# Performance work log

Hardware: AMD Instinct MI355X
Metric: run time of the kernel (lower is better)

## Reference

```python
import jax, jax.numpy as jnp
import numpy as np

HEADS, DIM_HEAD, LANDMARKS, PINV_ITERS = 8, 64, 256, 6


def moore_penrose_pinv(x, iters=PINV_ITERS):
    abs_x = jnp.abs(x)
    col = abs_x.sum(-1)
    row = abs_x.sum(-2)
    z = jnp.swapaxes(x, -1, -2) / (jnp.max(col) * jnp.max(row))
    I = jnp.eye(x.shape[-1], dtype=x.dtype)
    for _ in range(iters):
        xz = x @ z
        z = 0.25 * z @ (13 * I - xz @ (15 * I - xz @ (7 * I - xz)))
    return z


def nystrom_attention(x, w_qkv, w_out, b_out, res_conv_w):
    b, n, dim = x.shape
    m = LANDMARKS
    pad = (m - n % m) % m
    x = jnp.pad(x, ((0, 0), (pad, 0), (0, 0)))  # pad at front like F.pad(x,(0,0,pad,0))
    npad = n + pad
    qkv = x @ w_qkv  # (b, npad, 3*heads*dim_head)
    q, k, v = jnp.split(qkv, 3, axis=-1)
    sh = lambda t: t.reshape(b, npad, HEADS, DIM_HEAD).transpose(0, 2, 1, 3)
    q, k, v = sh(q), sh(k), sh(v)  # (b,h,npad,dh)
    q = q * (DIM_HEAD ** -0.5)
    l = npad // m
    q_l = q.reshape(b, HEADS, m, l, DIM_HEAD).mean(axis=3)  # landmarks (b,h,m,dh)
    k_l = k.reshape(b, HEADS, m, l, DIM_HEAD).mean(axis=3)
    attn1 = jax.nn.softmax(jnp.einsum('bhid,bhjd->bhij', q, k_l), -1)   # (b,h,npad,m)
    attn2 = jax.nn.softmax(jnp.einsum('bhid,bhjd->bhij', q_l, k_l), -1)  # (b,h,m,m)
    attn3 = jax.nn.softmax(jnp.einsum('bhid,bhjd->bhij', q_l, k), -1)   # (b,h,m,npad)
    out = attn1 @ (moore_penrose_pinv(attn2) @ (attn3 @ v))  # (b,h,npad,dh)
    # depthwise residual conv over sequence dim (Conv2d(heads,heads,(33,1),groups=heads,bias=False))
    res = jax.lax.conv_general_dilated(v, res_conv_w, (1, 1), ((16, 16), (0, 0)),
                                       dimension_numbers=('NCHW', 'OIHW', 'NCHW'),
                                       feature_group_count=HEADS)
    out = out + res
    out = out.transpose(0, 2, 1, 3).reshape(b, npad, HEADS * DIM_HEAD)
    out = out @ w_out + b_out
    return out[:, -n:]


def camil_forward(bag, adj_row, adj_col, adj_val, w_qkv, w_out, b_out, res_conv_w,
                  wq, wk, wv_w, wv_b, v_att, u_att, w_att, fc_kernel, fc_bias):
    N = bag.shape[1]
    # encoder
    xg = nystrom_attention(bag, w_qkv, w_out, b_out, res_conv_w)[0]  # (N,D)
    enc = xg + bag  # (1,N,D)
    q = enc @ wq  # (1,N,256)
    k = enc @ wk
    attn = jnp.einsum('bnd,bmd->bnm', q, k)[0] / jnp.sqrt(jnp.float32(256.0))  # (N,N)
    # sparse adjacency-masked neighbor aggregation
    edge_scores = adj_val * attn[adj_row, adj_col]
    A_raw = jax.ops.segment_sum(edge_scores, adj_row, num_segments=N)  # (N,)
    alpha = jax.nn.softmax(A_raw)
    value = bag @ wv_w + wv_b  # (1,N,D)
    xl = alpha[:, None] * value  # (1,N,D)
    wei2 = jax.nn.sigmoid(-xl) ** 2
    xo = xl * 2 * wei2 + 2 * enc * (1 - wei2)  # (1,N,D)
    # gated MIL attention (softmax over dim 0 of size 1, as in original)
    inst = jnp.tanh(xo @ v_att) * jax.nn.sigmoid(xo @ u_att)
    scores = inst @ w_att  # (1,N,1)
    k_alpha = jax.nn.softmax(scores, axis=0)
    attn_output = k_alpha * xo
    pooled = attn_output[0].sum(axis=0, keepdims=True)  # (1,D)
    out = pooled @ fc_kernel + fc_bias  # (1,1)
    return out, A_raw, k_alpha


def setup_inputs() -> dict:
    key = jax.random.key(0)
    ks = jax.random.split(key, 16)
    N, D, E = 10000, 512, 90000
    s = 0.02
    return {
        'bag': jax.random.normal(ks[0], (1, N, D), jnp.float32),
        'adj_row': jax.random.randint(ks[1], (E,), 0, N),
        'adj_col': jax.random.randint(ks[2], (E,), 0, N),
        'adj_val': jax.random.uniform(ks[3], (E,), jnp.float32),
        'w_qkv': jax.random.normal(ks[4], (D, 3 * HEADS * DIM_HEAD), jnp.float32) * s,
        'w_out': jax.random.normal(ks[5], (HEADS * DIM_HEAD, D), jnp.float32) * s,
        'b_out': jnp.zeros((D,), jnp.float32),
        'res_conv_w': jax.random.normal(ks[6], (HEADS, 1, 33, 1), jnp.float32) * s,
        'wq': jax.random.normal(ks[7], (D, 256), jnp.float32) * s,
        'wk': jax.random.normal(ks[8], (D, 256), jnp.float32) * s,
        'wv_w': jax.random.normal(ks[9], (D, D), jnp.float32) * s,
        'wv_b': jnp.zeros((D,), jnp.float32),
        'v_att': jax.random.normal(ks[10], (D, 128), jnp.float32) * s,
        'u_att': jax.random.normal(ks[11], (D, 128), jnp.float32) * s,
        'w_att': jax.random.normal(ks[12], (128, 1), jnp.float32) * s,
        'fc_kernel': jax.random.normal(ks[13], (D, 1), jnp.float32) * s,
        'fc_bias': jnp.zeros((1,), jnp.float32),
    }


def reference(bag, adj_row, adj_col, adj_val, w_qkv, w_out, b_out, res_conv_w,
              wq, wk, wv_w, wv_b, v_att, u_att, w_att, fc_kernel, fc_bias):
    return camil_forward(bag, adj_row, adj_col, adj_val, w_qkv, w_out, b_out, res_conv_w,
                         wq, wk, wv_w, wv_b, v_att, u_att, w_att, fc_kernel, fc_bias)
```

## Files before the change

kernel.cpp:

```cpp
#include <hip/hip_runtime.h>
#include <hip/hip_bf16.h>
#include <math.h>

#define NSEQ   10000
#define NPAD   10240
#define PADR   240
#define HEADS  8
#define DH     64
#define LM     256
#define LFAC   40
#define DMODEL 512
#define DQK    256
#define OUTSZ  20001
#define NSPLIT 16
#define KCH    128

typedef __attribute__((ext_vector_type(8))) short bf16x8;
typedef __attribute__((ext_vector_type(4))) float f32x4;
#define MFMA16(a,b,c) __builtin_amdgcn_mfma_f32_16x16x32_bf16(a,b,c,0,0,0)

typedef __attribute__((address_space(1))) const unsigned char gconst_t;
typedef __attribute__((address_space(3))) unsigned char lds_t;
#define GLD16(gp, lp) __builtin_amdgcn_global_load_lds((gconst_t*)(gp), (lds_t*)(lp), 16, 0, 0)

__device__ __forceinline__ float b2f(ushort u) {
    return __uint_as_float(((unsigned)u) << 16);
}
__device__ __forceinline__ ushort f2b(float f) {
    unsigned u = __float_as_uint(f);
    unsigned r = (u + 0x7FFFu + ((u >> 16) & 1u)) >> 16;
    return (ushort)r;
}
__device__ __forceinline__ unsigned fenc(float f) {
    unsigned u = __float_as_uint(f);
    return (u & 0x80000000u) ? ~u : (u | 0x80000000u);
}
__device__ __forceinline__ float fdec(unsigned k) {
    return __uint_as_float((k & 0x80000000u) ? (k & 0x7FFFFFFFu) : ~k);
}
__device__ __forceinline__ int swz8(int bid, int nwg) {
    int q = nwg >> 3, r = nwg & 7;
    int x = bid & 7, idx = bid >> 3;
    int start = (x < r) ? x * (q + 1) : r * (q + 1) + (x - r) * q;
    return start + idx;
}
__device__ __forceinline__ f32x4 tr4(f32x4 v, int p) {
    f32x4 u, w;
    float s, r;
    s = (p & 1) ? v[0] : v[1]; r = __shfl_xor(s, 1);
    u[0] = (p & 1) ? r : v[0]; u[1] = (p & 1) ? v[1] : r;
    s = (p & 1) ? v[2] : v[3]; r = __shfl_xor(s, 1);
    u[2] = (p & 1) ? r : v[2]; u[3] = (p & 1) ? v[3] : r;
    s = (p & 2) ? u[0] : u[2]; r = __shfl_xor(s, 2);
    w[0] = (p & 2) ? r : u[0]; w[2] = (p & 2) ? u[2] : r;
    s = (p & 2) ? u[1] : u[3]; r = __shfl_xor(s, 2);
    w[1] = (p & 2) ? r : u[1]; w[3] = (p & 2) ? u[3] : r;
    return w;
}

__global__ __launch_bounds__(256)
void cvtw_k(const float* __restrict__ in, ushort* __restrict__ out,
            float* __restrict__ outbuf, const float* __restrict__ fcb,
            unsigned int* __restrict__ mx,
            const float* __restrict__ w_qkv, const float* __restrict__ w_out,
            const float* __restrict__ wq, const float* __restrict__ wk,
            const float* __restrict__ wv_w,
            ushort* __restrict__ wqkvT, ushort* __restrict__ woutT,
            ushort* __restrict__ wqkT)
{
    __shared__ float tile[32][33];
    int bid = blockIdx.x;
    if (bid < 5000) {
        int i = bid * 256 + threadIdx.x;
        float4 v = ((const float4*)in)[i];
        ushort4 u; u.x = f2b(v.x); u.y = f2b(v.y); u.z = f2b(v.z); u.w = f2b(v.w);
        ((ushort4*)out)[i] = u;
        if (i == 0) {
            outbuf[0] = fcb[0];
            mx[0] = 0u; mx[1] = 0u;
            mx[2] = 0u;
            ((float*)mx)[3] = 0.f;
        }
        if (i >= 1 && i <= NSEQ) outbuf[i] = 0.f;
        if (i >= NSEQ + 1 && i < OUTSZ) outbuf[i] = 1.0f;
    } else {
        int wb = bid - 5000;
        int g0 = (wb % 96) * 32, r0 = (wb / 96) * 32;
        const float* src; ushort* outp; int C; int lc0;
        if (g0 < 1536)      { src = w_qkv; outp = wqkvT;                      C = 1536; lc0 = g0; }
        else if (g0 < 2048) { src = w_out; outp = woutT;                      C = 512;  lc0 = g0 - 1536; }
        else if (g0 < 2304) { src = wq;    outp = wqkT;                       C = 256;  lc0 = g0 - 2048; }
        else if (g0 < 2560) { src = wk;    outp = wqkT + 256*512;             C = 256;  lc0 = g0 - 2304; }
        else                { src = wv_w;  outp = wqkvT + (size_t)1536*512;   C = 512;  lc0 = g0 - 2560; }
        int tx = threadIdx.x & 31, ty = threadIdx.x >> 5;
        for (int i = ty; i < 32; i += 8) tile[i][tx] = src[(size_t)(r0 + i) * C + lc0 + tx];
        __syncthreads();
        for (int i = ty; i < 32; i += 8) outp[(size_t)(lc0 + i) * 512 + r0 + tx] = f2b(tile[tx][i]);
    }
}

template<int MODE, int TN>
__global__ __launch_bounds__(256)
void mgemm(const ushort* __restrict__ A, const ushort* __restrict__ Bt,
           int Mlog, int N, int K, int padr, int nbx,
           void* __restrict__ P0, void* __restrict__ P1, void* __restrict__ P2,
           void* __restrict__ P3, void* __restrict__ P4,
           const float* __restrict__ bias, const ushort* __restrict__ extra)
{
    constexpr int NF = TN / 32;
    constexpr int BSB = TN * 64;
    __shared__ __align__(16) char As[2 * 8192];
    __shared__ __align__(16) char Bs[2 * BSB];
    const int tid = threadIdx.x;
    const int l = tid & 63, w = tid >> 6;
    const int wm = w >> 1, wn = w & 1;
    const int wk_ = swz8(blockIdx.x, gridDim.x);
    const int row0 = (wk_ / nbx) * 128, col0 = (wk_ % nbx) * TN;
    const int lr = l & 15, lg = l >> 4;
    const bool slow = (MODE == 0) && (row0 < padr);
    const int NT = K >> 5;
    f32x4 acc[4][NF];
    #pragma unroll
    for (int i = 0; i < 4; ++i)
        #pragma unroll
        for (int j = 0; j < NF; ++j) acc[i][j] = (f32x4){0.f, 0.f, 0.f, 0.f};

    auto stage = [&](int bf, int t) {
        int k0 = t << 5;
        if (!slow) {
            #pragma unroll
            for (int c = 0; c < 2; ++c) {
                int q = w * 2 + c;
                int row = q * 16 + (l >> 2);
                GLD16(A + (size_t)(row0 + row - padr) * K + k0 + (l & 3) * 8,
                      As + bf * 8192 + q * 1024);
            }
            if (TN == 128) {
                #pragma unroll
                for (int c = 0; c < 2; ++c) {
                    int q = w * 2 + c;
                    int row = q * 16 + (l >> 2);
                    GLD16(Bt + (size_t)(col0 + row) * K + k0 + (l & 3) * 8,
                          Bs + bf * BSB + q * 1024);
                }
            } else {
                int row = w * 16 + (l >> 2);
                GLD16(Bt + (size_t)(col0 + row) * K + k0 + (l & 3) * 8,
                      Bs + bf * BSB + w * 1024);
            }
        } else {
            #pragma unroll
            for (int c = 0; c < 2; ++c) {
                int gidx = c * 256 + tid;
                int row = gidx >> 2, gr = gidx & 3;
                int phys = row0 + row - padr;
                uint4 v = {0, 0, 0, 0};
                if (phys >= 0 && phys < Mlog - padr)
                    v = *(const uint4*)(A + (size_t)phys * K + k0 + gr * 8);
                *(uint4*)(As + bf * 8192 + gidx * 16) = v;
            }
            if (TN == 128) {
                #pragma unroll
                for (int c = 0; c < 2; ++c) {
                    int gidx = c * 256 + tid;
                    int row = gidx >> 2, gr = gidx & 3;
                    *(uint4*)(Bs + bf * BSB + gidx * 16) =
                        *(const uint4*)(Bt + (size_t)(col0 + row) * K + k0 + gr * 8);
                }
            } else {
                int row = tid >> 2, gr = tid & 3;
                *(uint4*)(Bs + bf * BSB + tid * 16) =
                    *(const uint4*)(Bt + (size_t)(col0 + row) * K + k0 + gr * 8);
            }
        }
    };

    int cur = 0;
    stage(0, 0);
    __syncthreads();
    for (int t = 0; t < NT; ++t) {
        if (t + 1 < NT) stage(cur ^ 1, t + 1);
        const char* Ab = As + cur * 8192;
        const char* Bb = Bs + cur * BSB;
        bf16x8 af[4];
        #pragma unroll
        for (int mf = 0; mf < 4; ++mf)
            af[mf] = *(const bf16x8*)(Ab + (wm * 64 + mf * 16 + lr) * 64 + lg * 16);
        #pragma unroll
        for (int nf = 0; nf < NF; ++nf) {
            bf16x8 bfr = *(const bf16x8*)(Bb + (wn * (TN / 2) + nf * 16 + lr) * 64 + lg * 16);
            #pragma unroll
            for (int mf = 0; mf < 4; ++mf)
                acc[mf][nf] = MFMA16(af[mf], bfr, acc[mf][nf]);
        }
        __syncthreads();
        cur ^= 1;
    }

    const int p = lr & 3;
    #pragma unroll
    for (int mf = 0; mf < 4; ++mf)
    #pragma unroll
    for (int nf = 0; nf < NF; ++nf) {
        int cb   = col0 + wn * (TN / 2) + nf * 16 + (lr & 12);
        int rowT = row0 + wm * 64 + mf * 16 + lg * 4 + p;
        if (MODE == 0) {
            int c = col0 + wn * (TN / 2) + nf * 16 + lr;
            if ((c >> 9) == 2) {
                int hh = (c >> 6) & 7;
                int kt  = (row0 + wm * 64 + mf * 16 + lg * 4) >> 5;
                int lgp = ((mf * 2) + (lg >> 1)) & 3;
                int lanep = lr + lgp * 16;
                int e0 = (lg & 1) * 4;
                ushort4 pk;
                pk.x = f2b(acc[mf][nf][0]); pk.y = f2b(acc[mf][nf][1]);
                pk.z = f2b(acc[mf][nf][2]); pk.w = f2b(acc[mf][nf][3]);
                *(ushort4*)&((ushort*)P3)[(((size_t)hh * (NPAD/32) + kt) * 4 + (nf & 3)) * 512
                                          + lanep * 8 + e0] = pk;
            }
            int t = cb >> 9;
            f32x4 v = acc[mf][nf];
            if (t == 0) { v[0] *= 0.125f; v[1] *= 0.125f; v[2] *= 0.125f; v[3] *= 0.125f; }
            f32x4 wv = tr4(v, p);
            ushort4 pk;
            pk.x = f2b(wv[0]); pk.y = f2b(wv[1]); pk.z = f2b(wv[2]); pk.w = f2b(wv[3]);
            if (t < 3) {
                int hh = (cb >> 6) & 7, d0 = cb & 63;
                ushort* dst = (t == 0) ? (ushort*)P0 : (t == 1) ? (ushort*)P1 : (ushort*)P2;
                *(ushort4*)&dst[((size_t)hh * NPAD + rowT) * DH + d0] = pk;
            } else {
                int phys = rowT - PADR;
                if (phys >= 0)
                    *(ushort4*)&((ushort*)P4)[(size_t)phys * DMODEL + (cb & 511)] = pk;
            }
        } else if (MODE == 1) {
            f32x4 wv = tr4(acc[mf][nf], p);
            if (rowT < Mlog) {
                float4 bi = *(const float4*)(bias + cb);
                ushort4 bg = *(const ushort4*)(extra + (size_t)rowT * N + cb);
                float o0 = wv[0] + bi.x + b2f(bg.x), o1 = wv[1] + bi.y + b2f(bg.y);
                float o2 = wv[2] + bi.z + b2f(bg.z), o3 = wv[3] + bi.w + b2f(bg.w);
                ushort4 pk; pk.x = f2b(o0); pk.y = f2b(o1); pk.z = f2b(o2); pk.w = f2b(o3);
                *(ushort4*)&((ushort*)P1)[(size_t)rowT * N + cb] = pk;
            }
        } else if (MODE == 6) {
            f32x4 wv = tr4(acc[mf][nf], p);
            if (rowT < Mlog) {
                ushort4 pk;
                pk.x = f2b(wv[0]); pk.y = f2b(wv[1]); pk.z = f2b(wv[2]); pk.w = f2b(wv[3]);
                if (cb < 256)
                    *(ushort4*)&((ushort*)P0)[(size_t)rowT * 256 + cb] = pk;
                else
                    *(ushort4*)&((ushort*)P1)[(size_t)rowT * 256 + (cb - 256)] = pk;
            }
        }
    }
}

template<bool PLAIN, bool BCI, bool WPK>
__global__ __launch_bounds__(256)
void pinv_k(const ushort* __restrict__ A, const ushort* __restrict__ Bt,
            int N, float cval, float scale,
            ushort* __restrict__ P0, ushort* __restrict__ P1)
{
    __shared__ __align__(16) char smem[49152];
    char* As = smem;
    char* Bs = smem + 16384;
    const int tid = threadIdx.x, l = tid & 63, w = tid >> 6;
    const int lr = l & 15, lg = l >> 4;
    const int col0 = blockIdx.x * 64, row0 = blockIdx.y * 32, h = blockIdx.z;
    const ushort* Ab = A + (size_t)h * 65536;
    const ushort* Btb = Bt + (size_t)h * ((size_t)N * 256);
    {
        int row = tid >> 3, seg = (tid & 7) * 64;
        const uint4* sa = (const uint4*)(Ab + (size_t)(row0 + row) * 256) + (tid & 7) * 4;
        #pragma unroll
        for (int e = 0; e < 4; ++e) {
            int off = (row * 512 + seg + e * 16) ^ ((row & 7) << 4);
            *(uint4*)(As + off) = sa[e];
        }
    }
    {
        int row = tid >> 2, seg = (tid & 3) * 128;
        const uint4* sb = (const uint4*)(Btb + (size_t)(col0 + row) * 256) + (tid & 3) * 8;
        int gn = col0 + row;
        #pragma unroll
        for (int e = 0; e < 8; ++e) {
            int off = (row * 512 + seg + e * 16) ^ ((row & 7) << 4);
            uint4 vb = sb[e];
            if (BCI) {
                union { uint4 u; ushort s[8]; } t; t.u = vb;
                int gk0 = (seg >> 1) + e * 8;
                #pragma unroll
                for (int j = 0; j < 8; ++j)
                    t.s[j] = f2b(((gn == gk0 + j) ? cval : 0.f) - b2f(t.s[j]));
                vb = t.u;
            }
            *(uint4*)(Bs + off) = vb;
        }
    }
    __syncthreads();
    f32x4 acc[2];
    acc[0] = (f32x4){0.f, 0.f, 0.f, 0.f};
    acc[1] = (f32x4){0.f, 0.f, 0.f, 0.f};
    #pragma unroll
    for (int ks = 0; ks < 8; ++ks) {
        bf16x8 af[2];
        #pragma unroll
        for (int mf = 0; mf < 2; ++mf) {
            int ar = mf * 16 + lr;
            af[mf] = *(const bf16x8*)(As + ((ar * 512 + ks * 64 + lg * 16) ^ ((ar & 7) << 4)));
        }
        int br = w * 16 + lr;
        bf16x8 bf = *(const bf16x8*)(Bs + ((br * 512 + ks * 64 + lg * 16) ^ ((br & 7) << 4)));
        acc[0] = MFMA16(af[0], bf, acc[0]);
        acc[1] = MFMA16(af[1], bf, acc[1]);
    }
    #pragma unroll
    for (int mf = 0; mf < 2; ++mf) {
        int r0v = row0 + mf * 16 + lg * 4;
        int c = col0 + w * 16 + lr;
        if (PLAIN) {
            #pragma unroll
            for (int i = 0; i < 4; ++i)
                P0[(size_t)h * 256 * N + (size_t)(r0v + i) * N + c] = f2b(acc[mf][i] * scale);
        }
        ushort4 pk;
        pk.x = f2b(acc[mf][0] * scale); pk.y = f2b(acc[mf][1] * scale);
        pk.z = f2b(acc[mf][2] * scale); pk.w = f2b(acc[mf][3] * scale);
        if (WPK) {
            int off = (((c >> 4) * 8 + (r0v >> 5)) << 9) + (((r0v >> 3) & 3) << 7)
                    + ((c & 15) << 3) + (r0v & 4);
            *(ushort4*)&P1[(size_t)h * 16384 + off] = pk;
        } else {
            *(ushort4*)&P1[(size_t)h * ((size_t)N * 256) + (size_t)c * 256 + r0v] = pk;
        }
    }
}

__global__ __launch_bounds__(256)
void ns2_k(const ushort* __restrict__ P, const ushort* __restrict__ Pt,
           const ushort* __restrict__ Z,
           ushort* __restrict__ Qt, ushort* __restrict__ V1)
{
    __shared__ __align__(16) char smem[49152];
    char* As = smem;
    char* Bs = smem + 16384;
    const int tid = threadIdx.x, l = tid & 63, w = tid >> 6;
    const int lr = l & 15, lg = l >> 4;
    const int col0 = blockIdx.x * 64;
    const int which = blockIdx.y >> 3;
    const int row0 = (blockIdx.y & 7) * 32;
    const int h = blockIdx.z;
    const ushort* Ab = (which ? Z : P) + (size_t)h * 65536;
    const ushort* Btb = Pt + (size_t)h * 65536;
    {
        int row = tid >> 3, seg = (tid & 7) * 64;
        const uint4* sa = (const uint4*)(Ab + (size_t)(row0 + row) * 256) + (tid & 7) * 4;
        #pragma unroll
        for (int e = 0; e < 4; ++e) {
            int off = (row * 512 + seg + e * 16) ^ ((row & 7) << 4);
            *(uint4*)(As + off) = sa[e];
        }
    }
    {
        int row = tid >> 2, seg = (tid & 3) * 128;
        const uint4* sb = (const uint4*)(Btb + (size_t)(col0 + row) * 256) + (tid & 3) * 8;
        int gn = col0 + row;
        #pragma unroll
        for (int e = 0; e < 8; ++e) {
            int off = (row * 512 + seg + e * 16) ^ ((row & 7) << 4);
            uint4 vb = sb[e];
            if (which == 0) {
                union { uint4 u; ushort s[8]; } t; t.u = vb;
                int gk0 = (seg >> 1) + e * 8;
                #pragma unroll
                for (int j = 0; j < 8; ++j)
                    t.s[j] = f2b(((gn == gk0 + j) ? 7.f : 0.f) - b2f(t.s[j]));
                vb = t.u;
            }
            *(uint4*)(Bs + off) = vb;
        }
    }
    __syncthreads();
    f32x4 acc[2];
    acc[0] = (f32x4){0.f, 0.f, 0.f, 0.f};
    acc[1] = (f32x4){0.f, 0.f, 0.f, 0.f};
    #pragma unroll
    for (int ks = 0; ks < 8; ++ks) {
        bf16x8 af[2];
        #pragma unroll
        for (int mf = 0; mf < 2; ++mf) {
            int ar = mf * 16 + lr;
            af[mf] = *(const bf16x8*)(As + ((ar * 512 + ks * 64 + lg * 16) ^ ((ar & 7) << 4)));
        }
        int br = w * 16 + lr;
        bf16x8 bf = *(const bf16x8*)(Bs + ((br * 512 + ks * 64 + lg * 16) ^ ((br & 7) << 4)));
        acc[0] = MFMA16(af[0], bf, acc[0]);
        acc[1] = MFMA16(af[1], bf, acc[1]);
    }
    #pragma unroll
    for (int mf = 0; mf < 2; ++mf) {
        int r0v = row0 + mf * 16 + lg * 4;
        int c = col0 + w * 16 + lr;
        if (which == 0) {
            ushort4 pk;
            pk.x = f2b(acc[mf][0]); pk.y = f2b(acc[mf][1]);
            pk.z = f2b(acc[mf][2]); pk.w = f2b(acc[mf][3]);
            *(ushort4*)&Qt[(size_t)h * 65536 + (size_t)c * 256 + r0v] = pk;
        } else {
            #pragma unroll
            for (int i = 0; i < 4; ++i)
                V1[(size_t)h * 65536 + (size_t)(r0v + i) * 256 + c] = f2b(acc[mf][i]);
        }
    }
}

__global__ __launch_bounds__(256)
void ns3_k(const ushort* __restrict__ V1, const ushort* __restrict__ Qt,
           const ushort* __restrict__ Z,
           ushort* __restrict__ Zn, ushort* __restrict__ Znt)
{
    __shared__ __align__(16) char smem[49152];
    char* As = smem;
    char* Bs = smem + 16384;
    const int tid = threadIdx.x, l = tid & 63, w = tid >> 6;
    const int lr = l & 15, lg = l >> 4;
    const int col0 = blockIdx.x * 64, row0 = blockIdx.y * 32, h = blockIdx.z;
    const ushort* Ab = V1 + (size_t)h * 65536;
    const ushort* Btb = Qt + (size_t)h * 65536;
    {
        int row = tid >> 3, seg = (tid & 7) * 64;
        const uint4* sa = (const uint4*)(Ab + (size_t)(row0 + row) * 256) + (tid & 7) * 4;
        #pragma unroll
        for (int e = 0; e < 4; ++e) {
            int off = (row * 512 + seg + e * 16) ^ ((row & 7) << 4);
            *(uint4*)(As + off) = sa[e];
        }
    }
    {
        int row = tid >> 2, seg = (tid & 3) * 128;
        const uint4* sb = (const uint4*)(Btb + (size_t)(col0 + row) * 256) + (tid & 3) * 8;
        #pragma unroll
        for (int e = 0; e < 8; ++e) {
            int off = (row * 512 + seg + e * 16) ^ ((row & 7) << 4);
            *(uint4*)(Bs + off) = sb[e];
        }
    }
    __syncthreads();
    f32x4 acc[2];
    acc[0] = (f32x4){0.f, 0.f, 0.f, 0.f};
    acc[1] = (f32x4){0.f, 0.f, 0.f, 0.f};
    #pragma unroll
    for (int ks = 0; ks < 8; ++ks) {
        bf16x8 af[2];
        #pragma unroll
        for (int mf = 0; mf < 2; ++mf) {
            int ar = mf * 16 + lr;
            af[mf] = *(const bf16x8*)(As + ((ar * 512 + ks * 64 + lg * 16) ^ ((ar & 7) << 4)));
        }
        int br = w * 16 + lr;
        bf16x8 bf = *(const bf16x8*)(Bs + ((br * 512 + ks * 64 + lg * 16) ^ ((br & 7) << 4)));
        acc[0] = MFMA16(af[0], bf, acc[0]);
        acc[1] = MFMA16(af[1], bf, acc[1]);
    }
    #pragma unroll
    for (int mf = 0; mf < 2; ++mf) {
        int r0v = row0 + mf * 16 + lg * 4;
        int c = col0 + w * 16 + lr;
        ushort4 pk;
        #pragma unroll
        for (int i = 0; i < 4; ++i) {
            size_t idx = (size_t)h * 65536 + (size_t)(r0v + i) * 256 + c;
            float o = 0.25f * acc[mf][i] + 3.25f * b2f(Z[idx]) - 3.75f * b2f(V1[idx]);
            ushort u = f2b(o);
            Zn[idx] = u;
            ((ushort*)&pk)[i] = u;
        }
        *(ushort4*)&Znt[(size_t)h * 65536 + (size_t)c * 256 + r0v] = pk;
    }
}

__global__ __launch_bounds__(256)
void landconv_k(const ushort* __restrict__ Qb, const ushort* __restrict__ Kb,
                const ushort* __restrict__ Vb, const float* __restrict__ cw,
                ushort* __restrict__ OBc,
                ushort* __restrict__ QLb, ushort* __restrict__ KLb,
                ushort* __restrict__ KLpk)
{
    int bid = blockIdx.x;
    if (bid < 5000) {
        int idx = bid * 256 + threadIdx.x;
        int ro = idx >> 7, c4 = idx & 127;
        int h = c4 >> 4, dq = (c4 & 15) * 4;
        int i = ro + PADR;
        float a0 = 0, a1 = 0, a2 = 0, a3 = 0;
        #pragma unroll
        for (int tt = 0; tt < 33; ++tt) {
            int src = i + tt - 16;
            if (src < NPAD) {
                float wv = cw[h * 33 + tt];
                ushort4 u = *(const ushort4*)(Vb + ((size_t)h * NPAD + src) * DH + dq);
                a0 += wv * b2f(u.x); a1 += wv * b2f(u.y);
                a2 += wv * b2f(u.z); a3 += wv * b2f(u.w);
            }
        }
        ushort4 o; o.x = f2b(a0); o.y = f2b(a1); o.z = f2b(a2); o.w = f2b(a3);
        *(ushort4*)&OBc[(size_t)ro * DMODEL + h * DH + dq] = o;
    } else {
        int gidx = (bid - 5000) * 4 + (threadIdx.x >> 6);
        int d = threadIdx.x & 63;
        bool isK = gidx >= HEADS * LM;
        int b = isK ? gidx - HEADS * LM : gidx;
        int hh = b >> 8, j = b & 255;
        const ushort* p = (isK ? Kb : Qb) + ((size_t)hh * NPAD + (size_t)j * LFAC) * DH + d;
        float s = 0.f;
        #pragma unroll
        for (int t = 0; t < LFAC; ++t) s += b2f(p[t * DH]);
        ushort u = f2b(s * (1.f / LFAC));
        (isK ? KLb : QLb)[((size_t)hh * LM + j) * DH + d] = u;
        if (isK) {
            int nf = j >> 4, lr = j & 15;
            int ks = d >> 5, lg = (d >> 3) & 3, e = d & 7;
            KLpk[(((size_t)hh * 16 + nf) * 2 + ks) * 512 + (lg * 16 + lr) * 8 + e] = u;
        }
    }
}

__global__ __launch_bounds__(256)
void attn2m_k(const ushort* __restrict__ QLb, const ushort* __restrict__ KLpk,
              ushort* __restrict__ X2b)
{
    __shared__ __align__(16) char smem[40960];
    char*   Qs  = smem;
    ushort* KLs = (ushort*)(smem + 8192);
    const int tid = threadIdx.x, l = tid & 63, w = tid >> 6;
    const int h = blockIdx.y, i0 = blockIdx.x * 64;
    const int lr = l & 15, lg = l >> 4;
    {
        int row = tid >> 2;
        int seg = (tid & 3) * 32;
        const uint4* src = (const uint4*)(QLb + ((size_t)h * LM + i0 + row) * DH) + (tid & 3) * 2;
        uint4 v0 = src[0], v1 = src[1];
        int sw = (row & 7) << 4;
        *(uint4*)(Qs + row * 128 + (seg ^ sw)) = v0;
        *(uint4*)(Qs + row * 128 + ((seg + 16) ^ sw)) = v1;
    }
    {
        const uint4* src = (const uint4*)(KLpk + (size_t)h * 16384) + tid;
        uint4* dst = (uint4*)KLs + tid;
        #pragma unroll
        for (int e = 0; e < 8; ++e) dst[e * 256] = src[e * 256];
    }
    __syncthreads();

    f32x4 s[16];
    #pragma unroll
    for (int nf = 0; nf < 16; ++nf) s[nf] = (f32x4){0.f, 0.f, 0.f, 0.f};
    #pragma unroll
    for (int ks = 0; ks < 2; ++ks) {
        int qrow = w * 16 + lr;
        bf16x8 a = *(const bf16x8*)(Qs + qrow * 128 +
                                    ((ks * 64 + lg * 16) ^ ((qrow & 7) << 4)));
        #pragma unroll
        for (int nf = 0; nf < 16; ++nf) {
            bf16x8 b = *(const bf16x8*)&KLs[((nf * 2 + ks) * 64 + l) * 8];
            s[nf] = MFMA16(a, b, s[nf]);
        }
    }
    float inv_[4];
    #pragma unroll
    for (int i = 0; i < 4; ++i) {
        float m = s[0][i];
        #pragma unroll
        for (int nf = 1; nf < 16; ++nf) m = fmaxf(m, s[nf][i]);
        m = fmaxf(m, __shfl_xor(m, 1)); m = fmaxf(m, __shfl_xor(m, 2));
        m = fmaxf(m, __shfl_xor(m, 4)); m = fmaxf(m, __shfl_xor(m, 8));
        float sum = 0.f;
        #pragma unroll
        for (int nf = 0; nf < 16; ++nf) {
            float e = __expf(s[nf][i] - m); s[nf][i] = e; sum += e;
        }
        sum += __shfl_xor(sum, 1); sum += __shfl_xor(sum, 2);
        sum += __shfl_xor(sum, 4); sum += __shfl_xor(sum, 8);
        inv_[i] = 1.f / sum;
    }
    const int p = lr & 3;
    #pragma unroll
    for (int nf = 0; nf < 16; ++nf) {
        f32x4 v = s[nf];
        v[0] *= inv_[0]; v[1] *= inv_[1]; v[2] *= inv_[2]; v[3] *= inv_[3];
        f32x4 wv = tr4(v, p);
        int rowT = i0 + w * 16 + lg * 4 + p;
        int cb = nf * 16 + (lr & 12);
        ushort4 pk;
        pk.x = f2b(wv[0]); pk.y = f2b(wv[1]); pk.z = f2b(wv[2]); pk.w = f2b(wv[3]);
        *(ushort4*)&X2b[((size_t)h * LM + rowT) * LM + cb] = pk;
    }
}

__global__ __launch_bounds__(256)
void colrow_k(const ushort* __restrict__ X2b, unsigned int* __restrict__ mx)
{
    int h = blockIdx.x, t = threadIdx.x;
    const ushort* x = X2b + (size_t)h * LM * LM;
    float rs = 0.f;
    for (int i = 0; i < LM; ++i) rs += fabsf(b2f(x[(size_t)i * LM + t]));
    __shared__ float r2[256];
    r2[t] = rs; __syncthreads();
    for (int s = 128; s > 0; s >>= 1) {
        if (t < s) r2[t] = fmaxf(r2[t], r2[t + s]);
        __syncthreads();
    }
    if (t == 0) atomicMax(&mx[1], __float_as_uint(r2[0]));
}

__global__ void zinit_k(const ushort* __restrict__ X2b, const float* __restrict__ mxf,
                        ushort* __restrict__ Z, ushort* __restrict__ Zt)
{
    int i = blockIdx.x, h = blockIdx.y, j = threadIdx.x;
    float scale = 1.f / mxf[1];
    float x = b2f(X2b[((size_t)h * LM + i) * LM + j]) * scale;
    ushort u = f2b(x);
    Z[((size_t)h * LM + j) * LM + i] = u;
    Zt[((size_t)h * LM + i) * LM + j] = u;
}

__global__ __launch_bounds__(256)
void attn3_fa(const ushort* __restrict__ QLb, const ushort* __restrict__ Kb,
              const ushort* __restrict__ VtPk,
              float* __restrict__ Opart, float* __restrict__ Mpart,
              float* __restrict__ Lpart)
{
    __shared__ __align__(16) char smem[9216 + 18432];
    ushort* Qs = (ushort*)smem;
    ushort* Ks = (ushort*)(smem + 9216);
    ushort* Ps = (ushort*)(smem + 9216);
    const int tid = threadIdx.x, l = tid & 63, wv = tid >> 6;
    const int split = blockIdx.x, qt = blockIdx.y, h = blockIdx.z;
    const int lr = l & 15, lg = l >> 4;
    {
        int row = tid >> 2, seg = (tid & 3) * 16;
        const uint4* src = (const uint4*)(QLb + ((size_t)h * LM + qt * 64 + row) * DH + seg);
        *(uint4*)&Qs[row * 72 + seg] = src[0];
        *(uint4*)&Qs[row * 72 + seg + 8] = src[1];
    }
    f32x4 o[4];
    float m_[4], l_[4];
    #pragma unroll
    for (int nf = 0; nf < 4; ++nf) o[nf] = (f32x4){0.f, 0.f, 0.f, 0.f};
    #pragma unroll
    for (int i = 0; i < 4; ++i) { m_[i] = -INFINITY; l_[i] = 0.f; }
    const int k0base = split * (NPAD / NSPLIT);
    for (int ch = 0; ch < NPAD / NSPLIT / KCH; ++ch) {
        int kg0 = k0base + ch * KCH;
        __syncthreads();
        {
            int row = tid >> 1, half = (tid & 1) * 32;
            const uint4* src = (const uint4*)(Kb + ((size_t)h * NPAD + kg0 + row) * DH + half);
            #pragma unroll
            for (int e = 0; e < 4; ++e) *(uint4*)&Ks[row * 72 + half + e * 8] = src[e];
        }
        __syncthreads();
        f32x4 s[8];
        #pragma unroll
        for (int nf = 0; nf < 8; ++nf) s[nf] = (f32x4){0.f, 0.f, 0.f, 0.f};
        #pragma unroll
        for (int ks = 0; ks < 2; ++ks) {
            bf16x8 a = *(const bf16x8*)&Qs[(wv * 16 + lr) * 72 + ks * 32 + lg * 8];
            #pragma unroll
            for (int nf = 0; nf < 8; ++nf) {
                bf16x8 b = *(const bf16x8*)&Ks[(nf * 16 + lr) * 72 + ks * 32 + lg * 8];
                s[nf] = MFMA16(a, b, s[nf]);
            }
        }
        float scl[4];
        #pragma unroll
        for (int i = 0; i < 4; ++i) {
            float mx = s[0][i];
            #pragma unroll
            for (int nf = 1; nf < 8; ++nf) mx = fmaxf(mx, s[nf][i]);
            mx = fmaxf(mx, __shfl_xor(mx, 1)); mx = fmaxf(mx, __shfl_xor(mx, 2));
            mx = fmaxf(mx, __shfl_xor(mx, 4)); mx = fmaxf(mx, __shfl_xor(mx, 8));
            float mn = fmaxf(m_[i], mx);
            float sum = 0.f;
            #pragma unroll
            for (int nf = 0; nf < 8; ++nf) {
                float e = __expf(s[nf][i] - mn); s[nf][i] = e; sum += e;
            }
            sum += __shfl_xor(sum, 1); sum += __shfl_xor(sum, 2);
            sum += __shfl_xor(sum, 4); sum += __shfl_xor(sum, 8);
            float sc = __expf(m_[i] - mn);
            l_[i] = l_[i] * sc + sum;
            m_[i] = mn;
            scl[i] = sc;
        }
        #pragma unroll
        for (int nf = 0; nf < 4; ++nf)
        #pragma unroll
        for (int i = 0; i < 4; ++i) o[nf][i] *= scl[i];
        __syncthreads();
        #pragma unroll
        for (int nf = 0; nf < 8; ++nf)
        #pragma unroll
        for (int i = 0; i < 4; ++i) {
            int row = wv * 16 + lg * 4 + i;
            int col = nf * 16 + lr;
            Ps[row * 128 + (col ^ ((row & 7) << 3))] = f2b(s[nf][i]);
        }
        #pragma unroll
        for (int ks = 0; ks < 4; ++ks) {
            int row = wv * 16 + lr;
            int kcol = ks * 32 + lg * 8;
            bf16x8 a = *(const bf16x8*)&Ps[row * 128 + (kcol ^ ((row & 7) << 3))];
            int kgt = (kg0 >> 5) + ks;
            #pragma unroll
            for (int nf = 0; nf < 4; ++nf) {
                bf16x8 b = *(const bf16x8*)(VtPk +
                    (((size_t)h * (NPAD/32) + kgt) * 4 + nf) * 512 + (size_t)l * 8);
                o[nf] = MFMA16(a, b, o[nf]);
            }
        }
    }
    const int base = (split * 4 + qt) * 8 + h;
    #pragma unroll
    for (int nf = 0; nf < 4; ++nf)
    #pragma unroll
    for (int i = 0; i < 4; ++i) {
        int r = wv * 16 + lg * 4 + i;
        int c = nf * 16 + lr;
        Opart[((size_t)base * 64 + r) * 64 + c] = o[nf][i];
    }
    if (lr == 0) {
        #pragma unroll
        for (int i = 0; i < 4; ++i) {
            int r = wv * 16 + lg * 4 + i;
            Mpart[base * 64 + r] = m_[i];
            Lpart[base * 64 + r] = l_[i];
        }
    }
}

__global__ __launch_bounds__(256)
void mergeAV_k(const float* __restrict__ Opart, const float* __restrict__ Mpart,
               const float* __restrict__ Lpart, ushort* __restrict__ AVt)
{
    int qt = blockIdx.x, h = blockIdx.y, rq = blockIdx.z;
    int t = threadIdx.x;
    int r = rq * 32 + (t >> 3), c0 = (t & 7) * 8;
    float mv[NSPLIT];
    float mstar = -INFINITY;
    #pragma unroll
    for (int s = 0; s < NSPLIT; ++s) {
        mv[s] = Mpart[((s * 4 + qt) * 8 + h) * 64 + r];
        mstar = fmaxf(mstar, mv[s]);
    }
    float wgt[NSPLIT];
    float L = 0.f;
    #pragma unroll
    for (int s = 0; s < NSPLIT; ++s) {
        wgt[s] = __expf(mv[s] - mstar);
        L += wgt[s] * Lpart[((s * 4 + qt) * 8 + h) * 64 + r];
    }
    float inv = 1.f / L;
    float acc[8] = {};
    #pragma unroll
    for (int s = 0; s < NSPLIT; ++s) {
        const float* op = Opart + (((size_t)(s * 4 + qt) * 8 + h) * 64 + r) * 64 + c0;
        #pragma unroll
        for (int e = 0; e < 8; ++e) acc[e] += wgt[s] * op[e];
    }
    #pragma unroll
    for (int e = 0; e < 8; ++e)
        AVt[((size_t)h * DH + c0 + e) * LM + qt * 64 + r] = f2b(acc[e] * inv);
}

__global__ __launch_bounds__(256, 4)
void outrows64v2(const ushort* __restrict__ Qb, const ushort* __restrict__ KLpk,
                 const ushort* __restrict__ Wpk, const ushort* __restrict__ OBc,
                 ushort* __restrict__ OBb)
{
    __shared__ __align__(16) char smem[40960];
    char*   Qs  = smem;
    ushort* KLs = (ushort*)(smem + 8192);
    ushort* Ps  = (ushort*)(smem + 8192);
    const int tid = threadIdx.x, l = tid & 63, w = tid >> 6;
    const int h = blockIdx.y, i0 = blockIdx.x * 64;
    const int lr = l & 15, lg = l >> 4;

    ushort obc[4][4];
    #pragma unroll
    for (int nf = 0; nf < 4; ++nf)
    #pragma unroll
    for (int i = 0; i < 4; ++i) {
        int r = i0 + w * 16 + lg * 4 + i;
        obc[nf][i] = (r >= PADR)
            ? OBc[(size_t)(r - PADR) * DMODEL + h * DH + nf * 16 + lr] : (ushort)0;
    }
    {
        int row = tid >> 2;
        int seg = (tid & 3) * 32;
        const uint4* src = (const uint4*)(Qb + ((size_t)h * NPAD + i0 + row) * DH) + (tid & 3) * 2;
        uint4 v0 = src[0], v1 = src[1];
        int sw = (row & 7) << 4;
        *(uint4*)(Qs + row * 128 + (seg ^ sw)) = v0;
        *(uint4*)(Qs + row * 128 + ((seg + 16) ^ sw)) = v1;
    }
    {
        const uint4* src = (const uint4*)(KLpk + (size_t)h * 16384) + tid;
        uint4* dst = (uint4*)KLs + tid;
        #pragma unroll
        for (int e = 0; e < 8; ++e) dst[e * 256] = src[e * 256];
    }
    __syncthreads();

    f32x4 s[16];
    #pragma unroll
    for (int nf = 0; nf < 16; ++nf) s[nf] = (f32x4){0.f, 0.f, 0.f, 0.f};
    #pragma unroll
    for (int ks = 0; ks < 2; ++ks) {
        int qrow = w * 16 + lr;
        bf16x8 a = *(const bf16x8*)(Qs + qrow * 128 +
                                    ((ks * 64 + lg * 16) ^ ((qrow & 7) << 4)));
        #pragma unroll
        for (int nf = 0; nf < 16; ++nf) {
            bf16x8 b = *(const bf16x8*)&KLs[((nf * 2 + ks) * 64 + l) * 8];
            s[nf] = MFMA16(a, b, s[nf]);
        }
    }
    float inv_[4];
    #pragma unroll
    for (int i = 0; i < 4; ++i) {
        float m = s[0][i];
        #pragma unroll
        for (int nf = 1; nf < 16; ++nf) m = fmaxf(m, s[nf][i]);
        m = fmaxf(m, __shfl_xor(m, 1)); m = fmaxf(m, __shfl_xor(m, 2));
        m = fmaxf(m, __shfl_xor(m, 4)); m = fmaxf(m, __shfl_xor(m, 8));
        float sum = 0.f;
        #pragma unroll
        for (int nf = 0; nf < 16; ++nf) {
            float e = __expf(s[nf][i] - m); s[nf][i] = e; sum += e;
        }
        sum += __shfl_xor(sum, 1); sum += __shfl_xor(sum, 2);
        sum += __shfl_xor(sum, 4); sum += __shfl_xor(sum, 8);
        inv_[i] = 1.f / sum;
    }
    __syncthreads();
    #pragma unroll
    for (int nf = 0; nf < 16; ++nf)
    #pragma unroll
    for (int i = 0; i < 4; ++i) {
        int row = w * 16 + lg * 4 + i;
        int col = nf * 16 + lr;
        Ps[row * 256 + (col ^ ((row & 7) << 3))] = f2b(s[nf][i] * inv_[i]);
    }
    f32x4 o[4];
    #pragma unroll
    for (int nf = 0; nf < 4; ++nf) o[nf] = (f32x4){0.f, 0.f, 0.f, 0.f};
    #pragma unroll
    for (int ks = 0; ks < 8; ++ks) {
        int row = w * 16 + lr;
        int kcol = ks * 32 + lg * 8;
        bf16x8 a = *(const bf16x8*)&Ps[row * 256 + (kcol ^ ((row & 7) << 3))];
        #pragma unroll
        for (int nf = 0; nf < 4; ++nf) {
            bf16x8 b = *(const bf16x8*)(Wpk + (((size_t)h * 2048) + nf * 512 + ks * 64 + l) * 8);
            o[nf] = MFMA16(a, b, o[nf]);
        }
    }
    #pragma unroll
    for (int nf = 0; nf < 4; ++nf)
    #pragma unroll
    for (int i = 0; i < 4; ++i) {
        int r = i0 + w * 16 + lg * 4 + i;
        if (r >= PADR) {
            int ro = r - PADR;
            int c = h * DH + nf * 16 + lr;
            OBb[(size_t)ro * DMODEL + c] = f2b(o[nf][i] + b2f(obc[nf][i]));
        }
    }
}

__global__ __launch_bounds__(256)
void edges_k(const int* __restrict__ rows, const int* __restrict__ cols,
             const float* __restrict__ vals,
             const ushort* __restrict__ QE, const ushort* __restrict__ KE,
             float* __restrict__ A_raw, int E)
{
    int gid = blockIdx.x * blockDim.x + threadIdx.x;
    int e = gid >> 4, l = gid & 15;
    if (e >= E) return;
    int r = rows[e], c = cols[e];
    const uint4* qp = (const uint4*)(QE + (size_t)r * DQK + l * 16);
    const uint4* kp = (const uint4*)(KE + (size_t)c * DQK + l * 16);
    float dot = 0.f;
    #pragma unroll
    for (int g = 0; g < 2; ++g) {
        union { uint4 u; ushort s[8]; } qq, kk;
        qq.u = qp[g]; kk.u = kp[g];
        #pragma unroll
        for (int j = 0; j < 8; ++j) dot += b2f(qq.s[j]) * b2f(kk.s[j]);
    }
    dot += __shfl_xor(dot, 8); dot += __shfl_xor(dot, 4);
    dot += __shfl_xor(dot, 2); dot += __shfl_xor(dot, 1);
    if (l == 0) atomicAdd(&A_raw[r], vals[e] * dot * 0.0625f);
}

__global__ __launch_bounds__(256)
void amax_k(const float* __restrict__ A_raw, unsigned int* __restrict__ mx)
{
    __shared__ float red[256];
    int t = threadIdx.x;
    float lm = -INFINITY;
    for (int i = blockIdx.x * 256 + t; i < NSEQ; i += gridDim.x * 256)
        lm = fmaxf(lm, A_raw[i]);
    red[t] = lm; __syncthreads();
    for (int s = 128; s > 0; s >>= 1) { if (t < s) red[t] = fmaxf(red[t], red[t + s]); __syncthreads(); }
    if (t == 0) atomicMax(&mx[2], fenc(red[0]));
}

__global__ __launch_bounds__(256)
void aexp_k(const float* __restrict__ A_raw, const unsigned int* __restrict__ mx,
            float* __restrict__ alpha, float* __restrict__ sum)
{
    __shared__ float red[256];
    int t = threadIdx.x;
    float m = fdec(mx[2]);
    float ls = 0.f;
    for (int i = blockIdx.x * 256 + t; i < NSEQ; i += gridDim.x * 256) {
        float e = __expf(A_raw[i] - m);
        alpha[i] = e;
        ls += e;
    }
    red[t] = ls; __syncthreads();
    for (int s = 128; s > 0; s >>= 1) { if (t < s) red[t] += red[t + s]; __syncthreads(); }
    if (t == 0) atomicAdd(sum, red[0]);
}

__global__ __launch_bounds__(256)
void xo_pooled_k(const ushort* __restrict__ VALb, const ushort* __restrict__ ENCb,
                 const float* __restrict__ alpha, const float* __restrict__ asum,
                 const float* __restrict__ wvb, const float* __restrict__ fck,
                 float* __restrict__ out0)
{
    __shared__ float red[256];
    int t = threadIdx.x;
    float inv_sum = 1.f / asum[0];
    float acc = 0.f;
    const int total = NSEQ * 128;
    for (int idx = blockIdx.x * 256 + t; idx < total; idx += gridDim.x * 256) {
        int r = idx >> 7, dq = (idx & 127) * 4;
        float al = alpha[r] * inv_sum;
        ushort4 v4 = *(const ushort4*)(VALb + (size_t)r * DMODEL + dq);
        ushort4 e4 = *(const ushort4*)(ENCb + (size_t)r * DMODEL + dq);
        float4 b4 = *(const float4*)(wvb + dq);
        float4 f4 = *(const float4*)(fck + dq);
        float vv[4] = {b2f(v4.x) + b4.x, b2f(v4.y) + b4.y,
                       b2f(v4.z) + b4.z, b2f(v4.w) + b4.w};
        float ee[4] = {b2f(e4.x), b2f(e4.y), b2f(e4.z), b2f(e4.w)};
        float ff[4] = {f4.x, f4.y, f4.z, f4.w};
        #pragma unroll
        for (int j = 0; j < 4; ++j) {
            float xl = al * vv[j];
            float s = 1.f / (1.f + __expf(xl));
            float w2 = s * s;
            float xo = 2.f * xl * w2 + 2.f * ee[j] * (1.f - w2);
            acc += xo * ff[j];
        }
    }
    red[t] = acc; __syncthreads();
    for (int s = 128; s > 0; s >>= 1) { if (t < s) red[t] += red[t + s]; __syncthreads(); }
    if (t == 0) atomicAdd(out0, red[0]);
}

extern "C" void kernel_launch(void* const* d_in, const int* in_sizes, int n_in,
                              void* d_out, int out_size, void* d_ws, size_t ws_size,
                              hipStream_t stream)
{
    (void)n_in; (void)out_size; (void)ws_size;
    const float* bag   = (const float*)d_in[0];
    const int*   arow  = (const int*)d_in[1];
    const int*   acol  = (const int*)d_in[2];
    const float* aval  = (const float*)d_in[3];
    const float* w_qkv = (const float*)d_in[4];
    const float* w_out = (const float*)d_in[5];
    const float* b_out = (const float*)d_in[6];
    const float* convw = (const float*)d_in[7];
    const float* wq    = (const float*)d_in[8];
    const float* wk    = (const float*)d_in[9];
    const float* wv_w  = (const float*)d_in[10];
    const float* wv_b  = (const float*)d_in[11];
    const float* fck   = (const float*)d_in[15];
    const float* fcb   = (const float*)d_in[16];
    const int E = in_sizes[1];
    float* out = (float*)d_out;

    char* ws = (char*)d_ws;
    size_t off = 0;
    auto alloc = [&](size_t bytes) { void* p = ws + off; off += (bytes + 255) & ~(size_t)255; return p; };
    ushort* Qb    = (ushort*)alloc((size_t)HEADS * NPAD * DH * 2);
    ushort* Kb    = (ushort*)alloc((size_t)HEADS * NPAD * DH * 2);
    ushort* Vb    = (ushort*)alloc((size_t)HEADS * NPAD * DH * 2);
    ushort* bagb  = (ushort*)alloc((size_t)NSEQ * DMODEL * 2);
    ushort* wqkvT = (ushort*)alloc((size_t)2048 * 512 * 2);
    ushort* woutT = (ushort*)alloc((size_t)512 * 512 * 2);
    ushort* wqkT  = (ushort*)alloc((size_t)512 * 512 * 2);
    ushort* VALb  = (ushort*)alloc((size_t)NSEQ * DMODEL * 2);
    ushort* QLb   = (ushort*)alloc((size_t)HEADS * LM * DH * 2);
    ushort* KLb   = (ushort*)alloc((size_t)HEADS * LM * DH * 2);
    ushort* KLpk  = (ushort*)alloc((size_t)HEADS * LM * DH * 2);
    ushort* Wpk   = (ushort*)alloc((size_t)HEADS * DH * LM * 2);
    ushort* X2b   = (ushort*)alloc((size_t)HEADS * LM * LM * 2);
    ushort* Za    = (ushort*)alloc((size_t)HEADS * LM * LM * 2);
    ushort* Zat   = (ushort*)alloc((size_t)HEADS * LM * LM * 2);
    ushort* Zb2   = (ushort*)alloc((size_t)HEADS * LM * LM * 2);
    ushort* Zbt2  = (ushort*)alloc((size_t)HEADS * LM * LM * 2);
    ushort* T0    = (ushort*)alloc((size_t)HEADS * LM * LM * 2);
    ushort* T0t   = (ushort*)alloc((size_t)HEADS * LM * LM * 2);
    ushort* T1t   = (ushort*)alloc((size_t)HEADS * LM * LM * 2);
    ushort* T2t   = (ushort*)alloc((size_t)HEADS * LM * LM * 2);
    ushort* AVt   = (ushort*)alloc((size_t)HEADS * DH * LM * 2);
    ushort* OBc   = (ushort*)alloc((size_t)NSEQ * DMODEL * 2);
    ushort* OBb   = (ushort*)alloc((size_t)NSEQ * DMODEL * 2);
    float*  ENCf  = (float*)alloc((size_t)NSEQ * DMODEL * 4);
    ushort* ENCb  = (ushort*)alloc((size_t)NSEQ * DMODEL * 2);
    float*  ALPHA = (float*)alloc((size_t)NPAD * 4);
    float*  MXf   = (float*)alloc(256);
    unsigned int* MX = (unsigned int*)MXf;
    ushort* QEb = Qb;
    ushort* KEb = Kb;
    ushort* VtPk  = (ushort*)ENCf;
    float*  Opart = (float*)ENCb;
    float*  Mpart = (float*)((char*)ENCb + 8388608);
    float*  Lpart = (float*)((char*)ENCb + 8519680);

    cvtw_k<<<6536, 256, 0, stream>>>(bag, bagb, out, fcb, MX,
                                     w_qkv, w_out, wq, wk, wv_w,
                                     wqkvT, woutT, wqkT);

    mgemm<0, 128><<<1280, 256, 0, stream>>>(
        bagb, wqkvT, NPAD, 2048, 512, PADR, 16,
        Qb, Kb, Vb, VtPk, VALb, nullptr, nullptr);

    landconv_k<<<6024, 256, 0, stream>>>(Qb, Kb, Vb, convw, OBc, QLb, KLb, KLpk);

    attn2m_k<<<dim3(4, HEADS), 256, 0, stream>>>(QLb, KLpk, X2b);
    colrow_k<<<HEADS, 256, 0, stream>>>(X2b, MX);
    zinit_k<<<dim3(LM, HEADS), 256, 0, stream>>>(X2b, MXf, Za, Zat);

    ushort *Z = Za, *Zt = Zat, *Zn = Zb2, *Znt = Zbt2;
    for (int it = 0; it < 6; ++it) {
        pinv_k<true, false, false><<<dim3(4, 8, HEADS), 256, 0, stream>>>(
            X2b, Zt, LM, 0.f, 1.f, T0, T0t);
        ns2_k<<<dim3(4, 16, HEADS), 256, 0, stream>>>(T0, T0t, Z, T1t, T2t);
        ns3_k<<<dim3(4, 8, HEADS), 256, 0, stream>>>(T2t, T1t, Z, Zn, Znt);
        ushort* t;
        t = Z; Z = Zn; Zn = t;
        t = Zt; Zt = Znt; Znt = t;
    }

    attn3_fa<<<dim3(NSPLIT, 4, HEADS), 256, 0, stream>>>(QLb, Kb, VtPk, Opart, Mpart, Lpart);
    mergeAV_k<<<dim3(4, HEADS, 2), 256, 0, stream>>>(Opart, Mpart, Lpart, AVt);
    pinv_k<false, false, true><<<dim3(1, 8, HEADS), 256, 0, stream>>>(
        Za, AVt, DH, 0.f, 1.f, nullptr, Wpk);

    outrows64v2<<<dim3(NPAD / 64, HEADS), 256, 0, stream>>>(Qb, KLpk, Wpk, OBc, OBb);

    mgemm<1, 64><<<632, 256, 0, stream>>>(
        OBb, woutT, NSEQ, DMODEL, 512, 0, 8,
        nullptr, ENCb, nullptr, nullptr, nullptr, b_out, bagb);

    mgemm<6, 64><<<632, 256, 0, stream>>>(
        ENCb, wqkT, NSEQ, 512, 512, 0, 8,
        QEb, KEb, nullptr, nullptr, nullptr, nullptr, nullptr);

    edges_k<<<(E * 16 + 255) / 256, 256, 0, stream>>>(arow, acol, aval, QEb, KEb, out + 1, E);
    amax_k<<<40, 256, 0, stream>>>(out + 1, MX);
    aexp_k<<<40, 256, 0, stream>>>(out + 1, MX, ALPHA, MXf + 3);

    xo_pooled_k<<<1280, 256, 0, stream>>>(VALb, ENCb, ALPHA, MXf + 3, wv_b, fck, out);
}
```

Baseline: 337.7 us.

## Add 256x256-tile double-buffered QKV GEMM kernel for bulk rows

Adds a new 512-thread GEMM kernel with 256x256 output tiles, double-buffered LDS staging via direct global-to-LDS loads with XOR swizzle, and MFMA priority boosting. It handles all rows past the first 256-row band, while the original 128-tile kernel now runs only 32 blocks to cover the first band. The aim is more data reuse per block and better overlap of loads with MFMA work in the large QKV projection. The trade-off is 128KB of LDS per block, which limits occupancy, plus a duplicated epilogue that has to match the original output layouts exactly.

```diff
diff --git a/kernel.cpp b/kernel.cpp
--- a/kernel.cpp
+++ b/kernel.cpp
@@ -253,6 +253,137 @@
                 else
                     *(ushort4*)&((ushort*)P1)[(size_t)rowT * 256 + (cb - 256)] = pk;
             }
+        }
+    }
+}
+
+__global__ __launch_bounds__(512, 2)
+void mgemm8(const ushort* __restrict__ A, const ushort* __restrict__ Bt,
+            void* __restrict__ P0, void* __restrict__ P1, void* __restrict__ P2,
+            void* __restrict__ P3, void* __restrict__ P4)
+{
+    __shared__ __align__(16) char smem[131072];
+    const int tid = threadIdx.x;
+    const int l = tid & 63, w = tid >> 6;
+    const int wr = w >> 2, wc = w & 3;
+    const int lr = l & 15, lg = l >> 4;
+    const int wk_ = swz8(blockIdx.x, gridDim.x);
+    const int row0 = 256 + (wk_ >> 3) * 256;
+    const int col0 = (wk_ & 7) * 256;
+    const int rowA0 = row0 - PADR;
+
+    f32x4 acc[8][4];
+    #pragma unroll
+    for (int i = 0; i < 8; ++i)
+        #pragma unroll
+        for (int j = 0; j < 4; ++j) acc[i][j] = (f32x4){0.f, 0.f, 0.f, 0.f};
+
+    auto stage = [&](int bf, int t) {
+        int k0 = t << 6;
+        char* buf = smem + bf * 65536;
+        #pragma unroll
+        for (int i = 0; i < 4; ++i) {
+            int p = w * 4096 + i * 1024 + l * 16;
+            int row = p >> 7;
+            int sw = (p & 127) ^ ((row & 7) << 4);
+            int ke = k0 + (sw >> 1);
+            GLD16(A + (size_t)(rowA0 + row) * 512 + ke, buf + w * 4096 + i * 1024);
+            GLD16(Bt + (size_t)(col0 + row) * 512 + ke, buf + 32768 + w * 4096 + i * 1024);
+        }
+    };
+
+    stage(0, 0);
+    stage(1, 1);
+    asm volatile("s_waitcnt vmcnt(8)" ::: "memory");
+    __builtin_amdgcn_s_barrier();
+
+    #pragma unroll
+    for (int t = 0; t < 8; ++t) {
+        const int cur = t & 1;
+        const char* Ab = smem + cur * 65536;
+        const char* Bb = Ab + 32768;
+        bf16x8 a[8], b[4];
+        #pragma unroll
+        for (int mf = 0; mf < 8; ++mf) {
+            int r = wr * 128 + mf * 16 + lr;
+            a[mf] = *(const bf16x8*)(Ab + r * 128 + ((lg * 16) ^ ((r & 7) << 4)));
+        }
+        #pragma unroll
+        for (int nf = 0; nf < 4; ++nf) {
+            int cl = wc * 64 + nf * 16 + lr;
+            b[nf] = *(const bf16x8*)(Bb + cl * 128 + ((lg * 16) ^ ((cl & 7) << 4)));
+        }
+        __builtin_amdgcn_s_setprio(1);
+        #pragma unroll
+        for (int nf = 0; nf < 4; ++nf)
+            #pragma unroll
+            for (int mf = 0; mf < 8; ++mf)
+                acc[mf][nf] = MFMA16(a[mf], b[nf], acc[mf][nf]);
+        __builtin_amdgcn_s_setprio(0);
+        #pragma unroll
+        for (int mf = 0; mf < 8; ++mf) {
+            int r = wr * 128 + mf * 16 + lr;
+            a[mf] = *(const bf16x8*)(Ab + r * 128 + ((64 + lg * 16) ^ ((r & 7) << 4)));
+        }
+        #pragma unroll
+        for (int nf = 0; nf < 4; ++nf) {
+            int cl = wc * 64 + nf * 16 + lr;
+            b[nf] = *(const bf16x8*)(Bb + cl * 128 + ((64 + lg * 16) ^ ((cl & 7) << 4)));
+        }
+        if (t < 6) {
+            asm volatile("s_waitcnt lgkmcnt(0)" ::: "memory");
+            __builtin_amdgcn_s_barrier();
+            stage(cur, t + 2);
+        }
+        __builtin_amdgcn_s_setprio(1);
+        #pragma unroll
+        for (int nf = 0; nf < 4; ++nf)
+            #pragma unroll
+            for (int mf = 0; mf < 8; ++mf)
+                acc[mf][nf] = MFMA16(a[mf], b[nf], acc[mf][nf]);
+        __builtin_amdgcn_s_setprio(0);
+        if (t < 6) {
+            asm volatile("s_waitcnt vmcnt(8)" ::: "memory");
+            __builtin_amdgcn_s_barrier();
+        } else if (t == 6) {
+            asm volatile("s_waitcnt vmcnt(0)" ::: "memory");
+            __builtin_amdgcn_s_barrier();
+        }
+    }
+
+    const int p = lr & 3;
+    #pragma unroll
+    for (int mf = 0; mf < 8; ++mf)
+    #pragma unroll
+    for (int nf = 0; nf < 4; ++nf) {
+        int cb   = col0 + wc * 64 + nf * 16 + (lr & 12);
+        int rowT = row0 + wr * 128 + mf * 16 + lg * 4 + p;
+        int c = col0 + wc * 64 + nf * 16 + lr;
+        if ((c >> 9) == 2) {
+            int hh = (c >> 6) & 7;
+            int kt  = (row0 + wr * 128 + mf * 16 + lg * 4) >> 5;
+            int lgp = ((mf * 2) + (lg >> 1)) & 3;
+            int lanep = lr + lgp * 16;
+            int e0 = (lg & 1) * 4;
+            ushort4 pk;
+            pk.x = f2b(acc[mf][nf][0]); pk.y = f2b(acc[mf][nf][1]);
+            pk.z = f2b(acc[mf][nf][2]); pk.w = f2b(acc[mf][nf][3]);
+            *(ushort4*)&((ushort*)P3)[(((size_t)hh * (NPAD/32) + kt) * 4 + nf) * 512
+                                      + lanep * 8 + e0] = pk;
+        }
+        int tq = cb >> 9;
+        f32x4 v = acc[mf][nf];
+        if (tq == 0) { v[0] *= 0.125f; v[1] *= 0.125f; v[2] *= 0.125f; v[3] *= 0.125f; }
+        f32x4 wv = tr4(v, p);
+        ushort4 pk;
+        pk.x = f2b(wv[0]); pk.y = f2b(wv[1]); pk.z = f2b(wv[2]); pk.w = f2b(wv[3]);
+        if (tq < 3) {
+            int hh = (cb >> 6) & 7, d0 = cb & 63;
+            ushort* dst = (tq == 0) ? (ushort*)P0 : (tq == 1) ? (ushort*)P1 : (ushort*)P2;
+            *(ushort4*)&dst[((size_t)hh * NPAD + rowT) * DH + d0] = pk;
+        } else {
+            int phys = rowT - PADR;
+            *(ushort4*)&((ushort*)P4)[(size_t)phys * DMODEL + (cb & 511)] = pk;
         }
     }
 }
@@ -1038,9 +1169,10 @@
                                      w_qkv, w_out, wq, wk, wv_w,
                                      wqkvT, woutT, wqkT);
 
-    mgemm<0, 128><<<1280, 256, 0, stream>>>(
+    mgemm<0, 128><<<32, 256, 0, stream>>>(
         bagb, wqkvT, NPAD, 2048, 512, PADR, 16,
         Qb, Kb, Vb, VtPk, VALb, nullptr, nullptr);
+    mgemm8<<<312, 512, 0, stream>>>(bagb, wqkvT, Qb, Kb, Vb, VtPk, VALb);
 
     landconv_k<<<6024, 256, 0, stream>>>(Qb, Kb, Vb, convw, OBc, QLb, KLb, KLpk);
 
```

After: 366.1 us. 8.4% more time.
